# Performance work log

Measured on AMD Instinct MI355X. Metric: run time of the kernel, lower is better.

Reference implementation:

```python
import jax, jax.numpy as jnp
import numpy as np

N, D, H = 3072, 1152, 16
HD = D // H  # 72


def setup_inputs() -> dict:
    key = jax.random.key(0)
    ks = jax.random.split(key, 12)
    w = lambda k, shp: jax.random.normal(k, shp, dtype=jnp.float32) * 0.02
    return {
        "hidden_states": jax.random.normal(ks[0], (N, D), dtype=jnp.float32),
        "rotary_pos_emb": jax.random.normal(ks[1], (N, HD // 2), dtype=jnp.float32),
        "cu_seqlens": jnp.arange(5, dtype=jnp.int32) * (N // 4),
        "wq": w(ks[2], (D, D)), "bq": jnp.zeros((D,), jnp.float32),
        "wk": w(ks[3], (D, D)), "bk": jnp.zeros((D,), jnp.float32),
        "wv": w(ks[4], (D, D)), "bv": jnp.zeros((D,), jnp.float32),
        "wo": w(ks[5], (D, D)), "bo": jnp.zeros((D,), jnp.float32),
    }


def _rotate_half(x):
    x1, x2 = jnp.split(x, 2, axis=-1)
    return jnp.concatenate((-x2, x1), axis=-1)


def _apply_rope(t, freqs):
    # t: [N, H, HD], freqs: [N, HD//2]
    cos = jnp.concatenate([jnp.cos(freqs), jnp.cos(freqs)], axis=-1)[:, None, :]  # [N,1,HD]
    sin = jnp.concatenate([jnp.sin(freqs), jnp.sin(freqs)], axis=-1)[:, None, :]
    return (t.astype(jnp.float32) * cos + _rotate_half(t.astype(jnp.float32)) * sin).astype(t.dtype)


def reference(hidden_states, rotary_pos_emb, cu_seqlens, wq, bq, wk, bk, wv, bv, wo, bo):
    n = hidden_states.shape[0]
    q = (hidden_states @ wq.T + bq).reshape(n, H, HD)
    k = (hidden_states @ wk.T + bk).reshape(n, H, HD)
    v = (hidden_states @ wv.T + bv).reshape(n, H, HD)
    q = _apply_rope(q, rotary_pos_emb)
    k = _apply_rope(k, rotary_pos_emb)
    # block-diagonal mask: same segment id (from cu_seqlens) -> attend
    seg = jnp.searchsorted(cu_seqlens, jnp.arange(n), side="right")
    same = seg[:, None] == seg[None, :]  # [N, N]
    neg = jnp.finfo(q.dtype).min
    scores = jnp.einsum("qhd,khd->hqk", q, k) / jnp.sqrt(jnp.float32(HD)).astype(q.dtype)
    scores = scores + jnp.where(same, jnp.zeros((), q.dtype), neg)[None, :, :]
    attn = jax.nn.softmax(scores.astype(jnp.float32), axis=-1).astype(q.dtype)
    out = jnp.einsum("hqk,khd->qhd", attn, v).reshape(n, D)
    return out @ wo.T + bo
```

## Files before the change

kernel.cpp:

```cpp
#include <hip/hip_runtime.h>
#include <hip/hip_bf16.h>


typedef __attribute__((ext_vector_type(8))) __bf16 bf16x8;
typedef __attribute__((ext_vector_type(4))) float f32x4;
typedef __attribute__((ext_vector_type(8))) unsigned short u16x8;
typedef __attribute__((ext_vector_type(4))) unsigned short u16x4;

#define N_TOK 3072
#define DMODEL 1152
#define NH 16
#define HDIM 72
#define SEGLEN 768

__device__ __forceinline__ unsigned short bf16rn(float f) {
  union { float f; unsigned int u; } v; v.f = f;
  return (unsigned short)((v.u + 0x7fffu + ((v.u >> 16) & 1u)) >> 16);
}
__device__ __forceinline__ float bf2f(unsigned short u) {
  union { unsigned int i; float f; } v; v.i = ((unsigned int)u) << 16;
  return v.f;
}

#define GLOAD16(gsrc, ldst)                                                  \
  __builtin_amdgcn_global_load_lds(                                         \
      (const __attribute__((address_space(1))) unsigned int*)(gsrc),        \
      (__attribute__((address_space(3))) unsigned int*)(ldst), 16, 0, 0)

template <int N> __device__ __forceinline__ void waitcnt_vm() {
  if constexpr (N == 0) asm volatile("s_waitcnt vmcnt(0)" ::: "memory");
  else if constexpr (N == 2) asm volatile("s_waitcnt vmcnt(2)" ::: "memory");
  else if constexpr (N == 3) asm volatile("s_waitcnt vmcnt(3)" ::: "memory");
  else if constexpr (N == 4) asm volatile("s_waitcnt vmcnt(4)" ::: "memory");
}

__global__ __launch_bounds__(256) void prep_kernel(
    const float* __restrict__ hs,
    const float* __restrict__ wq, const float* __restrict__ wk,
    const float* __restrict__ wv, const float* __restrict__ wo,
    const float* __restrict__ bq, const float* __restrict__ bk,
    const float* __restrict__ bv,
    unsigned short* __restrict__ Xbf, unsigned short* __restrict__ Wqkv,
    unsigned short* __restrict__ Wo, float* __restrict__ biasqkv) {
  const int idx = blockIdx.x * 256 + threadIdx.x;
  const int stride = gridDim.x * 256;
  const int NX4 = (N_TOK * DMODEL) / 4;
  const int NW4 = (DMODEL * DMODEL) / 4;
  for (int i = idx; i < NX4; i += stride) {
    f32x4 v = ((const f32x4*)hs)[i];
    u16x4 o;
    for (int j = 0; j < 4; ++j) o[j] = bf16rn(v[j]);
    ((u16x4*)Xbf)[i] = o;
  }
  for (int i = idx; i < NW4; i += stride) {
    f32x4 a = ((const f32x4*)wq)[i];
    f32x4 b = ((const f32x4*)wk)[i];
    f32x4 c = ((const f32x4*)wv)[i];
    f32x4 d = ((const f32x4*)wo)[i];
    u16x4 oa, ob, oc, od;
    for (int j = 0; j < 4; ++j) {
      oa[j] = bf16rn(a[j]); ob[j] = bf16rn(b[j]);
      oc[j] = bf16rn(c[j]); od[j] = bf16rn(d[j]);
    }
    ((u16x4*)Wqkv)[i] = oa;
    ((u16x4*)(Wqkv + DMODEL * DMODEL))[i] = ob;
    ((u16x4*)(Wqkv + 2 * DMODEL * DMODEL))[i] = oc;
    ((u16x4*)Wo)[i] = od;
  }
  for (int i = idx; i < DMODEL; i += stride) {
    biasqkv[i] = bq[i];
    biasqkv[DMODEL + i] = bk[i];
    biasqkv[2 * DMODEL + i] = bv[i];
  }
}

template <int BM, int BN, int FM, int FN, bool OBF>
__global__ __launch_bounds__(256) void gemm_lds_kernel(
    const unsigned short* __restrict__ A, const unsigned short* __restrict__ B,
    const float* __restrict__ bias, void* __restrict__ Cout,
    int Nout, int K, int nbx) {
  __shared__ unsigned short As[3][BM * 32];
  __shared__ unsigned short Bs[3][BN * 32];
  const int t = threadIdx.x;
  const int lane = t & 63, wave = t >> 6;
  const int wr = wave >> 1, wc = wave & 1;
  const int g = lane >> 4, li = lane & 15;
  constexpr int LPS = BM / 64 + BN / 64;

  const int per = gridDim.x >> 3;
  const int gb = (blockIdx.x & 7) * per + (blockIdx.x >> 3);
  const int by = gb / nbx, bx = gb - by * nbx;
  const int bm = by * BM, bn = bx * BN;

  constexpr int LA = BM / 64;
  constexpr int LB = BN / 64;

  auto stage = [&](int buf, int kt) {
#pragma unroll
    for (int i = 0; i < LA; ++i) {
      const int s = i * 256 + t;
      const int row = s >> 2, cs = s & 3;
      const int gg = cs ^ ((row >> 1) & 3);
      GLOAD16(A + (long)(bm + row) * K + kt + gg * 8,
              &As[buf][(i * 256 + (t & ~63)) * 8]);
    }
#pragma unroll
    for (int i = 0; i < LB; ++i) {
      const int s = i * 256 + t;
      const int row = s >> 2, cs = s & 3;
      const int gg = cs ^ ((row >> 1) & 3);
      GLOAD16(B + (long)(bn + row) * K + kt + gg * 8,
              &Bs[buf][(i * 256 + (t & ~63)) * 8]);
    }
  };

  f32x4 acc[FM][FN];
#pragma unroll
  for (int i = 0; i < FM; ++i)
#pragma unroll
    for (int j = 0; j < FN; ++j) acc[i][j] = (f32x4)0.f;

  stage(0, 0);
  stage(1, 32);
  int cur = 0;
  const int nk = K / 32;
  for (int kt = 0; kt < nk; ++kt) {
    if (kt < nk - 1) waitcnt_vm<LPS>();
    else waitcnt_vm<0>();
    __builtin_amdgcn_s_barrier();
    __builtin_amdgcn_sched_barrier(0);
    if (kt + 2 < nk) {
      int nb = cur + 2; if (nb >= 3) nb -= 3;
      stage(nb, (kt + 2) * 32);
      __builtin_amdgcn_sched_barrier(0);
    }
    bf16x8 af[FM], bf[FN];
#pragma unroll
    for (int i = 0; i < FM; ++i) {
      const int r = wr * (BM / 2) + i * 16 + li;
      af[i] = *(const bf16x8*)&As[cur][r * 32 + ((g ^ ((r >> 1) & 3)) * 8)];
    }
#pragma unroll
    for (int j = 0; j < FN; ++j) {
      const int r = wc * (BN / 2) + j * 16 + li;
      bf[j] = *(const bf16x8*)&Bs[cur][r * 32 + ((g ^ ((r >> 1) & 3)) * 8)];
    }
    __builtin_amdgcn_s_setprio(1);
#pragma unroll
    for (int i = 0; i < FM; ++i)
#pragma unroll
      for (int j = 0; j < FN; ++j)
        acc[i][j] = __builtin_amdgcn_mfma_f32_16x16x32_bf16(af[i], bf[j],
                                                            acc[i][j], 0, 0, 0);
    __builtin_amdgcn_s_setprio(0);
    cur = (cur == 2) ? 0 : cur + 1;
  }

#pragma unroll
  for (int i = 0; i < FM; ++i) {
    const int row = bm + wr * (BM / 2) + i * 16 + g * 4;
#pragma unroll
    for (int j = 0; j < FN; ++j) {
      const int col = bn + wc * (BN / 2) + j * 16 + li;
      const float bb = bias[col];
#pragma unroll
      for (int r = 0; r < 4; ++r) {
        const float v = acc[i][j][r] + bb;
        if constexpr (OBF)
          ((unsigned short*)Cout)[(long)(row + r) * Nout + col] = bf16rn(v);
        else
          ((float*)Cout)[(long)(row + r) * Nout + col] = v;
      }
    }
  }
}

__global__ __launch_bounds__(256) void rope_pack_kernel(
    const unsigned short* __restrict__ qkv, const float* __restrict__ rope,
    unsigned short* __restrict__ Qp, unsigned short* __restrict__ Kp,
    unsigned short* __restrict__ Vt) {
  const int nb = blockIdx.x;
  const int h = blockIdx.y;
  const int n0 = nb * 64;
  const int t = threadIdx.x;
  const float qscale = 0.17002501f;
  __shared__ float cs[64][36], sn[64][36];
  __shared__ float vtile[72][65];

  for (int i = t; i < 64 * 36; i += 256) {
    const int n = i / 36, d = i % 36;
    const float f = rope[(long)(n0 + n) * 36 + d];
    cs[n][d] = __cosf(f);
    sn[n][d] = __sinf(f);
  }
  __syncthreads();

  for (int i = t; i < 64 * 9; i += 256) {
    const int n = i / 9, dq = (i % 9) * 4;
    const long base = (long)(n0 + n) * 3456 + h * HDIM;
    u16x4 q1 = *(const u16x4*)&qkv[base + dq];
    u16x4 q2 = *(const u16x4*)&qkv[base + dq + 36];
    u16x4 k1 = *(const u16x4*)&qkv[base + DMODEL + dq];
    u16x4 k2 = *(const u16x4*)&qkv[base + DMODEL + dq + 36];
    u16x4 oq1, oq2, ok1, ok2;
#pragma unroll
    for (int e = 0; e < 4; ++e) {
      const float c = cs[n][dq + e], s = sn[n][dq + e];
      float f1 = bf2f(q1[e]), f2 = bf2f(q2[e]);
      oq1[e] = bf16rn((f1 * c - f2 * s) * qscale);
      oq2[e] = bf16rn((f2 * c + f1 * s) * qscale);
      f1 = bf2f(k1[e]); f2 = bf2f(k2[e]);
      ok1[e] = bf16rn(f1 * c - f2 * s);
      ok2[e] = bf16rn(f2 * c + f1 * s);
    }
    const long ob = ((long)h * N_TOK + n0 + n) * 96;
    *(u16x4*)&Qp[ob + dq] = oq1;
    *(u16x4*)&Qp[ob + dq + 36] = oq2;
    *(u16x4*)&Kp[ob + dq] = ok1;
    *(u16x4*)&Kp[ob + dq + 36] = ok2;
  }
  for (int i = t; i < 64 * 6; i += 256) {
    const int n = i / 6, dp = HDIM + (i % 6) * 4;
    const long ob = ((long)h * N_TOK + n0 + n) * 96;
    *(u16x4*)&Qp[ob + dp] = (u16x4)0;
    *(u16x4*)&Kp[ob + dp] = (u16x4)0;
  }
  for (int i = t; i < 64 * 9; i += 256) {
    const int n = i / 9, dq = (i % 9) * 8;
    u16x8 v = *(const u16x8*)&qkv[(long)(n0 + n) * 3456 + 2 * DMODEL + h * HDIM + dq];
#pragma unroll
    for (int e = 0; e < 8; ++e) vtile[dq + e][n] = bf2f(v[e]);
  }
  __syncthreads();
  for (int i = t; i < 80 * 8; i += 256) {
    const int d = i / 8, nq = (i % 8) * 8;
    u16x8 o;
#pragma unroll
    for (int e = 0; e < 8; ++e)
      o[e] = (d < HDIM) ? bf16rn(vtile[d][nq + e])
                        : (d == HDIM ? (unsigned short)0x3F80
                                     : (unsigned short)0);
    *(u16x8*)&Vt[((long)h * 80 + d) * N_TOK + n0 + nq] = o;
  }
}

__global__ __launch_bounds__(256) void attn_kernel(
    const unsigned short* __restrict__ Qp, const unsigned short* __restrict__ Kp,
    const unsigned short* __restrict__ Vt, unsigned short* __restrict__ pO,
    float* __restrict__ pl) {
  const int b = blockIdx.x;
  const int hs = b & 63, u = b >> 6;
  const int h = hs >> 2, seg = hs & 3;
  const int qt = u >> 1, half = u & 1;
  const int t = threadIdx.x;
  const int lane = t & 63, w = t >> 6;
  const int g = lane >> 4, li = lane & 15;

  __shared__ unsigned short Ks[2][32 * 96];
  __shared__ unsigned short Vs[2][80 * 32];
  __shared__ unsigned short Ps[4][16][48];

  const int q0 = seg * SEGLEN + qt * 64;
  const int koff0 = half * 384;
  const unsigned short* kbase = Kp + ((long)h * N_TOK + seg * SEGLEN) * 96;
  const unsigned short* vbase = Vt + (long)h * 80 * N_TOK + seg * SEGLEN;

  auto stageK = [&](int buf, int koff) {
    {
      const int row = t / 12, c = t - row * 12;
      const int gg = c ^ ((row >> 1) & 3);
      GLOAD16(kbase + (long)(koff + row) * 96 + gg * 8,
              &Ks[buf][(t & ~63) * 8]);
    }
    if (t < 128) {
      const int s = 256 + t;
      const int row = s / 12, c = s - row * 12;
      const int gg = c ^ ((row >> 1) & 3);
      GLOAD16(kbase + (long)(koff + row) * 96 + gg * 8,
              &Ks[buf][(256 + (t & ~63)) * 8]);
    }
  };
  auto stageV = [&](int buf, int koff) {
    {
      const int row = t >> 2, ch = t & 3;
      const int gg = ch ^ ((row >> 1) & 3);
      GLOAD16(vbase + (long)row * N_TOK + koff + gg * 8,
              &Vs[buf][(t & ~63) * 8]);
    }
    if (t < 64) {
      const int s = 256 + t;
      const int row = s >> 2, ch = s & 3;
      const int gg = ch ^ ((row >> 1) & 3);
      GLOAD16(vbase + (long)row * N_TOK + koff + gg * 8,
              &Vs[buf][(256 + (t & ~63)) * 8]);
    }
  };

  bf16x8 aq[3];
  {
    const unsigned short* qsrc = Qp + ((long)h * N_TOK + q0 + w * 16 + li) * 96;
#pragma unroll
    for (int c = 0; c < 3; ++c)
      aq[c] = *(const bf16x8*)(qsrc + c * 32 + g * 8);
  }

  f32x4 accO[5];
#pragma unroll
  for (int j = 0; j < 5; ++j) accO[j] = (f32x4)0.f;

  stageK(0, koff0);
  stageV(0, koff0);
  int cur = 0;
  for (int kv = 0; kv < 12; ++kv) {
    __syncthreads();
    if (kv + 1 < 12) {
      stageK(cur ^ 1, koff0 + (kv + 1) * 32);
      stageV(cur ^ 1, koff0 + (kv + 1) * 32);
    }

    f32x4 sc[2];
#pragma unroll
    for (int f = 0; f < 2; ++f) sc[f] = (f32x4)0.f;
    __builtin_amdgcn_s_setprio(1);
#pragma unroll
    for (int c = 0; c < 3; ++c)
#pragma unroll
      for (int f = 0; f < 2; ++f) {
        const int kr = f * 16 + li;
        bf16x8 bk = *(const bf16x8*)
            &Ks[cur][kr * 96 + (((c * 4 + g) ^ ((kr >> 1) & 3)) * 8)];
        sc[f] = __builtin_amdgcn_mfma_f32_16x16x32_bf16(bk, aq[c], sc[f], 0, 0, 0);
      }
    __builtin_amdgcn_s_setprio(0);

#pragma unroll
    for (int f = 0; f < 2; ++f) {
      u16x4 pk;
#pragma unroll
      for (int r = 0; r < 4; ++r) pk[r] = bf16rn(exp2f(sc[f][r]));
      *(u16x4*)&Ps[w][li][f * 16 + g * 4] = pk;
    }

    {
      bf16x8 ap = *(const bf16x8*)&Ps[w][li][g * 8];
      __builtin_amdgcn_s_setprio(1);
#pragma unroll
      for (int j = 0; j < 5; ++j) {
        const int vr = j * 16 + li;
        bf16x8 bv = *(const bf16x8*)
            &Vs[cur][vr * 32 + ((g ^ ((vr >> 1) & 3)) * 8)];
        accO[j] = __builtin_amdgcn_mfma_f32_16x16x32_bf16(ap, bv, accO[j], 0, 0, 0);
      }
      __builtin_amdgcn_s_setprio(0);
    }
    cur ^= 1;
  }

  const long pbase = ((long)(half * 16 + h)) * N_TOK;
#pragma unroll
  for (int j = 0; j < 5; ++j) {
    const int d = j * 16 + li;
#pragma unroll
    for (int r = 0; r < 4; ++r) {
      const int n = q0 + w * 16 + g * 4 + r;
      pO[(pbase + n) * 80 + d] = bf16rn(accO[j][r]);
    }
  }
  if (li == 8) {
#pragma unroll
    for (int r = 0; r < 4; ++r)
      pl[pbase + q0 + w * 16 + g * 4 + r] = accO[4][r];
  }
}

__global__ __launch_bounds__(256) void combine_kernel(
    const unsigned short* __restrict__ pO, const float* __restrict__ pl,
    unsigned short* __restrict__ AO) {
  const int idx = blockIdx.x * 256 + threadIdx.x;
  const int row = idx / 9, q = idx - row * 9;
  const long HS = (long)NH * N_TOK * 80;
  u16x8 a = *(const u16x8*)&pO[(long)row * 80 + q * 8];
  u16x8 b = *(const u16x8*)&pO[HS + (long)row * 80 + q * 8];
  const float linv = 1.f / (pl[row] + pl[NH * N_TOK + row]);
  const int h = row / N_TOK, n = row - h * N_TOK;
  u16x8 o;
#pragma unroll
  for (int e = 0; e < 8; ++e)
    o[e] = bf16rn((bf2f(a[e]) + bf2f(b[e])) * linv);
  *(u16x8*)&AO[(long)n * DMODEL + h * HDIM + q * 8] = o;
}

extern "C" void kernel_launch(void* const* d_in, const int* in_sizes, int n_in,
                              void* d_out, int out_size, void* d_ws,
                              size_t ws_size, hipStream_t stream) {
  const float* hs = (const float*)d_in[0];
  const float* rope = (const float*)d_in[1];
  const float* wq = (const float*)d_in[3];
  const float* bq = (const float*)d_in[4];
  const float* wk = (const float*)d_in[5];
  const float* bk = (const float*)d_in[6];
  const float* wv = (const float*)d_in[7];
  const float* bv = (const float*)d_in[8];
  const float* wo = (const float*)d_in[9];
  const float* bo = (const float*)d_in[10];
  float* out = (float*)d_out;
  char* ws = (char*)d_ws;

  unsigned short* Xbf = (unsigned short*)(ws + 0);
  unsigned short* Wqkv = (unsigned short*)(ws + 7077888);
  unsigned short* Wo = (unsigned short*)(ws + 15040512);
  float* biasqkv = (float*)(ws + 17694720);
  unsigned short* qkvb = (unsigned short*)(ws + 17708544);
  unsigned short* pO = (unsigned short*)(ws + 17708544);
  float* pl = (float*)(ws + 33437184);
  unsigned short* Qp = (unsigned short*)(ws + 38942208);
  unsigned short* Kp = (unsigned short*)(ws + 48379392);
  unsigned short* Vt = (unsigned short*)(ws + 57816576);
  unsigned short* AO = (unsigned short*)(ws + 65680896);

  prep_kernel<<<dim3(1024), dim3(256), 0, stream>>>(
      hs, wq, wk, wv, wo, bq, bk, bv, Xbf, Wqkv, Wo, biasqkv);
  gemm_lds_kernel<128, 128, 4, 4, true><<<dim3(648), dim3(256), 0, stream>>>(
      Xbf, Wqkv, biasqkv, qkvb, 3 * DMODEL, DMODEL, 27);
  rope_pack_kernel<<<dim3(48, 16), dim3(256), 0, stream>>>(
      qkvb, rope, Qp, Kp, Vt);
  attn_kernel<<<dim3(1536), dim3(256), 0, stream>>>(Qp, Kp, Vt, pO, pl);
  combine_kernel<<<dim3(1728), dim3(256), 0, stream>>>(pO, pl, AO);
  gemm_lds_kernel<64, 128, 2, 4, false><<<dim3(432), dim3(256), 0, stream>>>(
      AO, Wo, bo, out, DMODEL, DMODEL, 9);
}
```

Before: 117.4 us.

## Add dedicated 192x128-tile QKV GEMM with BK=64 double buffering and interleaved prefetch

Replaces the generic 128x128 templated GEMM for the QKV projection with a specialised kernel using 192x128 tiles, K-step 64, and two LDS buffers. Global-to-LDS loads for the next tile are interleaved between MFMA groups, and s_setprio raises wave priority around the MFMA bursts. The grid shrinks from 648 to 432 blocks, which gives more reuse per tile and fewer K iterations. In exchange each block uses more LDS and registers (24 accumulators), which lowers occupancy, and 432 blocks may fill the CUs less evenly.

```diff
diff --git a/kernel.cpp b/kernel.cpp
--- a/kernel.cpp
+++ b/kernel.cpp
@@ -74,6 +74,159 @@
   }
 }
 
+__global__ __launch_bounds__(256) void gemm_qkv_kernel(
+    const unsigned short* __restrict__ A, const unsigned short* __restrict__ B,
+    const float* __restrict__ bias, unsigned short* __restrict__ C) {
+  constexpr int K = DMODEL;
+  constexpr int NOUT = 3 * DMODEL;
+  __shared__ unsigned short As[2][192 * 64];
+  __shared__ unsigned short Bs[2][128 * 64];
+  const int t = threadIdx.x;
+  const int lane = t & 63;
+  const int wave = t >> 6;
+  const int wr = wave >> 1, wc = wave & 1;
+  const int g = lane >> 4, li = lane & 15;
+
+  const int gb = (blockIdx.x & 7) * 54 + (blockIdx.x >> 3);
+  const int by = gb / 27, bx = gb - by * 27;
+  const int bm = by * 192, bn = bx * 128;
+
+  auto stageA = [&](int buf, int ko, int grp) {
+#pragma unroll
+    for (int i = 0; i < 2; ++i) {
+      const int s = grp * 512 + i * 256 + t;
+      const int row = s >> 3, ch = s & 7;
+      GLOAD16(A + (long)(bm + row) * K + ko + ((ch ^ (row & 7)) * 8),
+              &As[buf][(grp * 512 + i * 256 + (t & ~63)) * 8]);
+    }
+  };
+  auto stageB = [&](int buf, int ko, int grp) {
+#pragma unroll
+    for (int i = 0; i < 2; ++i) {
+      const int s = grp * 512 + i * 256 + t;
+      const int row = s >> 3, ch = s & 7;
+      GLOAD16(B + (long)(bn + row) * K + ko + ((ch ^ (row & 7)) * 8),
+              &Bs[buf][(grp * 512 + i * 256 + (t & ~63)) * 8]);
+    }
+  };
+  auto rdA = [&](int buf, int i, int ks) -> bf16x8 {
+    const int r = wr * 96 + i * 16 + li;
+    return *(const bf16x8*)&As[buf][r * 64 + ((((ks << 2) + g) ^ (r & 7)) * 8)];
+  };
+  auto rdB = [&](int buf, int j, int ks) -> bf16x8 {
+    const int r = wc * 64 + j * 16 + li;
+    return *(const bf16x8*)&Bs[buf][r * 64 + ((((ks << 2) + g) ^ (r & 7)) * 8)];
+  };
+
+  f32x4 acc[6][4];
+#pragma unroll
+  for (int i = 0; i < 6; ++i)
+#pragma unroll
+    for (int j = 0; j < 4; ++j) acc[i][j] = (f32x4)0.f;
+
+  stageA(0, 0, 0); stageA(0, 0, 1); stageA(0, 0, 2);
+  stageB(0, 0, 0); stageB(0, 0, 1);
+
+  for (int kt = 0; kt < 18; ++kt) {
+    const int buf = kt & 1;
+    const bool pf = kt < 17;
+    const int ko = (kt + 1) * 64;
+    if (pf) { stageA(buf ^ 1, ko, 0); waitcnt_vm<2>(); }
+    else waitcnt_vm<0>();
+    __builtin_amdgcn_s_barrier();
+
+    bf16x8 b0, b1, b2, b3, a0, a1;
+    b0 = rdB(buf, 0, 0); b1 = rdB(buf, 1, 0);
+    b2 = rdB(buf, 2, 0); b3 = rdB(buf, 3, 0);
+    a0 = rdA(buf, 0, 0); a1 = rdA(buf, 1, 0);
+    if (pf) stageA(buf ^ 1, ko, 1);
+    __builtin_amdgcn_s_setprio(1);
+    acc[0][0] = __builtin_amdgcn_mfma_f32_16x16x32_bf16(a0, b0, acc[0][0], 0, 0, 0);
+    acc[0][1] = __builtin_amdgcn_mfma_f32_16x16x32_bf16(a0, b1, acc[0][1], 0, 0, 0);
+    acc[0][2] = __builtin_amdgcn_mfma_f32_16x16x32_bf16(a0, b2, acc[0][2], 0, 0, 0);
+    acc[0][3] = __builtin_amdgcn_mfma_f32_16x16x32_bf16(a0, b3, acc[0][3], 0, 0, 0);
+    acc[1][0] = __builtin_amdgcn_mfma_f32_16x16x32_bf16(a1, b0, acc[1][0], 0, 0, 0);
+    acc[1][1] = __builtin_amdgcn_mfma_f32_16x16x32_bf16(a1, b1, acc[1][1], 0, 0, 0);
+    acc[1][2] = __builtin_amdgcn_mfma_f32_16x16x32_bf16(a1, b2, acc[1][2], 0, 0, 0);
+    acc[1][3] = __builtin_amdgcn_mfma_f32_16x16x32_bf16(a1, b3, acc[1][3], 0, 0, 0);
+    __builtin_amdgcn_s_setprio(0);
+    a0 = rdA(buf, 2, 0); a1 = rdA(buf, 3, 0);
+    if (pf) stageA(buf ^ 1, ko, 2);
+    __builtin_amdgcn_s_setprio(1);
+    acc[2][0] = __builtin_amdgcn_mfma_f32_16x16x32_bf16(a0, b0, acc[2][0], 0, 0, 0);
+    acc[2][1] = __builtin_amdgcn_mfma_f32_16x16x32_bf16(a0, b1, acc[2][1], 0, 0, 0);
+    acc[2][2] = __builtin_amdgcn_mfma_f32_16x16x32_bf16(a0, b2, acc[2][2], 0, 0, 0);
+    acc[2][3] = __builtin_amdgcn_mfma_f32_16x16x32_bf16(a0, b3, acc[2][3], 0, 0, 0);
+    acc[3][0] = __builtin_amdgcn_mfma_f32_16x16x32_bf16(a1, b0, acc[3][0], 0, 0, 0);
+    acc[3][1] = __builtin_amdgcn_mfma_f32_16x16x32_bf16(a1, b1, acc[3][1], 0, 0, 0);
+    acc[3][2] = __builtin_amdgcn_mfma_f32_16x16x32_bf16(a1, b2, acc[3][2], 0, 0, 0);
+    acc[3][3] = __builtin_amdgcn_mfma_f32_16x16x32_bf16(a1, b3, acc[3][3], 0, 0, 0);
+    __builtin_amdgcn_s_setprio(0);
+    a0 = rdA(buf, 4, 0); a1 = rdA(buf, 5, 0);
+    if (pf) stageB(buf ^ 1, ko, 0);
+    __builtin_amdgcn_s_setprio(1);
+    acc[4][0] = __builtin_amdgcn_mfma_f32_16x16x32_bf16(a0, b0, acc[4][0], 0, 0, 0);
+    acc[4][1] = __builtin_amdgcn_mfma_f32_16x16x32_bf16(a0, b1, acc[4][1], 0, 0, 0);
+    acc[4][2] = __builtin_amdgcn_mfma_f32_16x16x32_bf16(a0, b2, acc[4][2], 0, 0, 0);
+    acc[4][3] = __builtin_amdgcn_mfma_f32_16x16x32_bf16(a0, b3, acc[4][3], 0, 0, 0);
+    acc[5][0] = __builtin_amdgcn_mfma_f32_16x16x32_bf16(a1, b0, acc[5][0], 0, 0, 0);
+    acc[5][1] = __builtin_amdgcn_mfma_f32_16x16x32_bf16(a1, b1, acc[5][1], 0, 0, 0);
+    acc[5][2] = __builtin_amdgcn_mfma_f32_16x16x32_bf16(a1, b2, acc[5][2], 0, 0, 0);
+    acc[5][3] = __builtin_amdgcn_mfma_f32_16x16x32_bf16(a1, b3, acc[5][3], 0, 0, 0);
+    __builtin_amdgcn_s_setprio(0);
+    b0 = rdB(buf, 0, 1); b1 = rdB(buf, 1, 1);
+    b2 = rdB(buf, 2, 1); b3 = rdB(buf, 3, 1);
+    a0 = rdA(buf, 0, 1); a1 = rdA(buf, 1, 1);
+    if (pf) stageB(buf ^ 1, ko, 1);
+    __builtin_amdgcn_s_setprio(1);
+    acc[0][0] = __builtin_amdgcn_mfma_f32_16x16x32_bf16(a0, b0, acc[0][0], 0, 0, 0);
+    acc[0][1] = __builtin_amdgcn_mfma_f32_16x16x32_bf16(a0, b1, acc[0][1], 0, 0, 0);
+    acc[0][2] = __builtin_amdgcn_mfma_f32_16x16x32_bf16(a0, b2, acc[0][2], 0, 0, 0);
+    acc[0][3] = __builtin_amdgcn_mfma_f32_16x16x32_bf16(a0, b3, acc[0][3], 0, 0, 0);
+    acc[1][0] = __builtin_amdgcn_mfma_f32_16x16x32_bf16(a1, b0, acc[1][0], 0, 0, 0);
+    acc[1][1] = __builtin_amdgcn_mfma_f32_16x16x32_bf16(a1, b1, acc[1][1], 0, 0, 0);
+    acc[1][2] = __builtin_amdgcn_mfma_f32_16x16x32_bf16(a1, b2, acc[1][2], 0, 0, 0);
+    acc[1][3] = __builtin_amdgcn_mfma_f32_16x16x32_bf16(a1, b3, acc[1][3], 0, 0, 0);
+    __builtin_amdgcn_s_setprio(0);
+    a0 = rdA(buf, 2, 1); a1 = rdA(buf, 3, 1);
+    __builtin_amdgcn_s_setprio(1);
+    acc[2][0] = __builtin_amdgcn_mfma_f32_16x16x32_bf16(a0, b0, acc[2][0], 0, 0, 0);
+    acc[2][1] = __builtin_amdgcn_mfma_f32_16x16x32_bf16(a0, b1, acc[2][1], 0, 0, 0);
+    acc[2][2] = __builtin_amdgcn_mfma_f32_16x16x32_bf16(a0, b2, acc[2][2], 0, 0, 0);
+    acc[2][3] = __builtin_amdgcn_mfma_f32_16x16x32_bf16(a0, b3, acc[2][3], 0, 0, 0);
+    acc[3][0] = __builtin_amdgcn_mfma_f32_16x16x32_bf16(a1, b0, acc[3][0], 0, 0, 0);
+    acc[3][1] = __builtin_amdgcn_mfma_f32_16x16x32_bf16(a1, b1, acc[3][1], 0, 0, 0);
+    acc[3][2] = __builtin_amdgcn_mfma_f32_16x16x32_bf16(a1, b2, acc[3][2], 0, 0, 0);
+    acc[3][3] = __builtin_amdgcn_mfma_f32_16x16x32_bf16(a1, b3, acc[3][3], 0, 0, 0);
+    __builtin_amdgcn_s_setprio(0);
+    a0 = rdA(buf, 4, 1); a1 = rdA(buf, 5, 1);
+    __builtin_amdgcn_s_setprio(1);
+    acc[4][0] = __builtin_amdgcn_mfma_f32_16x16x32_bf16(a0, b0, acc[4][0], 0, 0, 0);
+    acc[4][1] = __builtin_amdgcn_mfma_f32_16x16x32_bf16(a0, b1, acc[4][1], 0, 0, 0);
+    acc[4][2] = __builtin_amdgcn_mfma_f32_16x16x32_bf16(a0, b2, acc[4][2], 0, 0, 0);
+    acc[4][3] = __builtin_amdgcn_mfma_f32_16x16x32_bf16(a0, b3, acc[4][3], 0, 0, 0);
+    acc[5][0] = __builtin_amdgcn_mfma_f32_16x16x32_bf16(a1, b0, acc[5][0], 0, 0, 0);
+    acc[5][1] = __builtin_amdgcn_mfma_f32_16x16x32_bf16(a1, b1, acc[5][1], 0, 0, 0);
+    acc[5][2] = __builtin_amdgcn_mfma_f32_16x16x32_bf16(a1, b2, acc[5][2], 0, 0, 0);
+    acc[5][3] = __builtin_amdgcn_mfma_f32_16x16x32_bf16(a1, b3, acc[5][3], 0, 0, 0);
+    __builtin_amdgcn_s_setprio(0);
+    __builtin_amdgcn_s_barrier();
+  }
+
+#pragma unroll
+  for (int i = 0; i < 6; ++i) {
+    const int row = bm + wr * 96 + i * 16 + g * 4;
+#pragma unroll
+    for (int j = 0; j < 4; ++j) {
+      const int col = bn + wc * 64 + j * 16 + li;
+      const float bb = bias[col];
+#pragma unroll
+      for (int r = 0; r < 4; ++r)
+        C[(long)(row + r) * NOUT + col] = bf16rn(acc[i][j][r] + bb);
+    }
+  }
+}
+
 template <int BM, int BN, int FM, int FN, bool OBF>
 __global__ __launch_bounds__(256) void gemm_lds_kernel(
     const unsigned short* __restrict__ A, const unsigned short* __restrict__ B,
@@ -420,8 +573,8 @@
 
   prep_kernel<<<dim3(1024), dim3(256), 0, stream>>>(
       hs, wq, wk, wv, wo, bq, bk, bv, Xbf, Wqkv, Wo, biasqkv);
-  gemm_lds_kernel<128, 128, 4, 4, true><<<dim3(648), dim3(256), 0, stream>>>(
-      Xbf, Wqkv, biasqkv, qkvb, 3 * DMODEL, DMODEL, 27);
+  gemm_qkv_kernel<<<dim3(432), dim3(256), 0, stream>>>(
+      Xbf, Wqkv, biasqkv, qkvb);
   rope_pack_kernel<<<dim3(48, 16), dim3(256), 0, stream>>>(
       qkvb, rope, Qp, Kp, Vt);
   attn_kernel<<<dim3(1536), dim3(256), 0, stream>>>(Qp, Kp, Vt, pO, pl);
```

Result: slower. 120.5 us (+2.6%).

## Drop split-KV attention and combine kernel; normalize output inside attention

Applied to the files above, without the earlier changes.

The attention kernel no longer splits each segment's keys into two halves. Each block now loops over all 24 KV tiles and normalizes its output using the row-sum column taken from the V ones-row, then writes bf16 results straight into AO. This removes the combine kernel launch and the partial-output and partial-sum round trip through global memory. In exchange it halves the attention grid to 768 blocks, which lowers parallelism and makes each block's serial loop twice as long. Separately, the sched_barrier hints around staging in the GEMM main loop are removed, leaving instruction placement to the compiler.

```diff
diff --git a/kernel.cpp b/kernel.cpp
--- a/kernel.cpp
+++ b/kernel.cpp
@@ -128,11 +128,9 @@
     if (kt < nk - 1) waitcnt_vm<LPS>();
     else waitcnt_vm<0>();
     __builtin_amdgcn_s_barrier();
-    __builtin_amdgcn_sched_barrier(0);
     if (kt + 2 < nk) {
       int nb = cur + 2; if (nb >= 3) nb -= 3;
       stage(nb, (kt + 2) * 32);
-      __builtin_amdgcn_sched_barrier(0);
     }
     bf16x8 af[FM], bf[FN];
 #pragma unroll
@@ -246,12 +244,10 @@
 
 __global__ __launch_bounds__(256) void attn_kernel(
     const unsigned short* __restrict__ Qp, const unsigned short* __restrict__ Kp,
-    const unsigned short* __restrict__ Vt, unsigned short* __restrict__ pO,
-    float* __restrict__ pl) {
+    const unsigned short* __restrict__ Vt, unsigned short* __restrict__ AO) {
   const int b = blockIdx.x;
-  const int hs = b & 63, u = b >> 6;
+  const int hs = b & 63, qt = b >> 6;
   const int h = hs >> 2, seg = hs & 3;
-  const int qt = u >> 1, half = u & 1;
   const int t = threadIdx.x;
   const int lane = t & 63, w = t >> 6;
   const int g = lane >> 4, li = lane & 15;
@@ -261,7 +257,6 @@
   __shared__ unsigned short Ps[4][16][48];
 
   const int q0 = seg * SEGLEN + qt * 64;
-  const int koff0 = half * 384;
   const unsigned short* kbase = Kp + ((long)h * N_TOK + seg * SEGLEN) * 96;
   const unsigned short* vbase = Vt + (long)h * 80 * N_TOK + seg * SEGLEN;
 
@@ -308,14 +303,14 @@
 #pragma unroll
   for (int j = 0; j < 5; ++j) accO[j] = (f32x4)0.f;
 
-  stageK(0, koff0);
-  stageV(0, koff0);
+  stageK(0, 0);
+  stageV(0, 0);
   int cur = 0;
-  for (int kv = 0; kv < 12; ++kv) {
+  for (int kv = 0; kv < 24; ++kv) {
     __syncthreads();
-    if (kv + 1 < 12) {
-      stageK(cur ^ 1, koff0 + (kv + 1) * 32);
-      stageV(cur ^ 1, koff0 + (kv + 1) * 32);
+    if (kv + 1 < 24) {
+      stageK(cur ^ 1, (kv + 1) * 32);
+      stageV(cur ^ 1, (kv + 1) * 32);
     }
 
     f32x4 sc[2];
@@ -356,38 +351,23 @@
     cur ^= 1;
   }
 
-  const long pbase = ((long)(half * 16 + h)) * N_TOK;
+  float rinv[4];
+#pragma unroll
+  for (int r = 0; r < 4; ++r)
+    rinv[r] = 1.f / __shfl(accO[4][r], (lane & 48) + 8);
+
+  const int hb = h * HDIM;
 #pragma unroll
   for (int j = 0; j < 5; ++j) {
     const int d = j * 16 + li;
-#pragma unroll
-    for (int r = 0; r < 4; ++r) {
-      const int n = q0 + w * 16 + g * 4 + r;
-      pO[(pbase + n) * 80 + d] = bf16rn(accO[j][r]);
-    }
-  }
-  if (li == 8) {
-#pragma unroll
-    for (int r = 0; r < 4; ++r)
-      pl[pbase + q0 + w * 16 + g * 4 + r] = accO[4][r];
-  }
-}
-
-__global__ __launch_bounds__(256) void combine_kernel(
-    const unsigned short* __restrict__ pO, const float* __restrict__ pl,
-    unsigned short* __restrict__ AO) {
-  const int idx = blockIdx.x * 256 + threadIdx.x;
-  const int row = idx / 9, q = idx - row * 9;
-  const long HS = (long)NH * N_TOK * 80;
-  u16x8 a = *(const u16x8*)&pO[(long)row * 80 + q * 8];
-  u16x8 b = *(const u16x8*)&pO[HS + (long)row * 80 + q * 8];
-  const float linv = 1.f / (pl[row] + pl[NH * N_TOK + row]);
-  const int h = row / N_TOK, n = row - h * N_TOK;
-  u16x8 o;
-#pragma unroll
-  for (int e = 0; e < 8; ++e)
-    o[e] = bf16rn((bf2f(a[e]) + bf2f(b[e])) * linv);
-  *(u16x8*)&AO[(long)n * DMODEL + h * HDIM + q * 8] = o;
+    if (d < HDIM) {
+#pragma unroll
+      for (int r = 0; r < 4; ++r) {
+        const int n = q0 + w * 16 + g * 4 + r;
+        AO[(long)n * DMODEL + hb + d] = bf16rn(accO[j][r] * rinv[r]);
+      }
+    }
+  }
 }
 
 extern "C" void kernel_launch(void* const* d_in, const int* in_sizes, int n_in,
@@ -411,8 +391,6 @@
   unsigned short* Wo = (unsigned short*)(ws + 15040512);
   float* biasqkv = (float*)(ws + 17694720);
   unsigned short* qkvb = (unsigned short*)(ws + 17708544);
-  unsigned short* pO = (unsigned short*)(ws + 17708544);
-  float* pl = (float*)(ws + 33437184);
   unsigned short* Qp = (unsigned short*)(ws + 38942208);
   unsigned short* Kp = (unsigned short*)(ws + 48379392);
   unsigned short* Vt = (unsigned short*)(ws + 57816576);
@@ -424,8 +402,7 @@
       Xbf, Wqkv, biasqkv, qkvb, 3 * DMODEL, DMODEL, 27);
   rope_pack_kernel<<<dim3(48, 16), dim3(256), 0, stream>>>(
       qkvb, rope, Qp, Kp, Vt);
-  attn_kernel<<<dim3(1536), dim3(256), 0, stream>>>(Qp, Kp, Vt, pO, pl);
-  combine_kernel<<<dim3(1728), dim3(256), 0, stream>>>(pO, pl, AO);
+  attn_kernel<<<dim3(768), dim3(256), 0, stream>>>(Qp, Kp, Vt, AO);
   gemm_lds_kernel<64, 128, 2, 4, false><<<dim3(432), dim3(256), 0, stream>>>(
       AO, Wo, bo, out, DMODEL, DMODEL, 9);
 }
```

After: 110.3 us. -6.1%, faster.
